# Optimization experiments

Measured on AMD Instinct MI355X. Metric: run time of the kernel, lower is better.

Reference implementation:

```python
import jax, jax.numpy as jnp
import numpy as np
from jax import lax

KH = KW = 3
DIL = 4
D = DIL * (KH - 1) + 1  # dilated (effective) kernel extent = 9
PAD = 4
STRIDE = 1


def setup_inputs() -> dict:
    key = jax.random.key(0)
    k1, k2, k3, k4 = jax.random.split(key, 4)
    Cin, Cout, B, H, W = 128, 128, 16, 112, 112
    fan_in = Cin * KH * KW
    x = jax.random.normal(k1, (B, Cin, H, W), dtype=jnp.float32)
    weight = jax.random.normal(k2, (Cout, Cin, KH, KW), dtype=jnp.float32) / np.sqrt(fan_in)
    # learnable positions: offsets of each kernel point inside the dilated kernel
    P = jax.random.normal(k3, (2, Cout, Cin, KH, KW), dtype=jnp.float32) * (DIL / 2.0)
    bias = jax.random.normal(k4, (Cout,), dtype=jnp.float32) * 0.01
    return {"x": x, "weight": weight, "P": P, "bias": bias}


def _construct_kernel(weight, P):
    # Place each kernel point at its (learnable) continuous position inside the
    # D x D dilated kernel via bilinear interpolation (DCLS construction).
    O, C, kh, kw = weight.shape
    base_h = jnp.arange(kh, dtype=weight.dtype) * DIL  # regular dilated grid
    base_w = jnp.arange(kw, dtype=weight.dtype) * DIL
    p_h = jnp.clip(base_h[None, None, :, None] + P[0], 0.0, D - 1)  # (O,C,kh,kw)
    p_w = jnp.clip(base_w[None, None, None, :] + P[1], 0.0, D - 1)
    fh = jnp.floor(p_h)
    fw = jnp.floor(p_w)
    rh = p_h - fh  # fractional residuals -> bilinear weights
    rw = p_w - fw
    ih = fh.astype(jnp.int32)
    iw = fw.astype(jnp.int32)
    ih1 = jnp.minimum(ih + 1, D - 1)
    iw1 = jnp.minimum(iw + 1, D - 1)
    o = jnp.arange(O)[:, None, None, None]
    c = jnp.arange(C)[None, :, None, None]
    K = jnp.zeros((O, C, D, D), dtype=weight.dtype)
    K = K.at[o, c, ih, iw].add(weight * (1 - rh) * (1 - rw))
    K = K.at[o, c, ih1, iw].add(weight * rh * (1 - rw))
    K = K.at[o, c, ih, iw1].add(weight * (1 - rh) * rw)
    K = K.at[o, c, ih1, iw1].add(weight * rh * rw)
    return K


def reference(x, weight, P, bias):
    K = _construct_kernel(weight, P)  # (Cout, Cin, D, D)
    out = lax.conv_general_dilated(
        x, K,
        window_strides=(STRIDE, STRIDE),
        padding=[(PAD, PAD), (PAD, PAD)],
        dimension_numbers=("NCHW", "OIHW", "NCHW"),
        feature_group_count=1,
    )
    return out + bias[None, :, None, None]
```

## Files before the change

### kernel.cpp

```cpp
#include <hip/hip_runtime.h>
#include <hip/hip_bf16.h>
#include <stdint.h>


typedef __attribute__((ext_vector_type(8))) short short8;
typedef __attribute__((ext_vector_type(16))) float f32x16;

__device__ inline unsigned short f2bf(float f) {
    union { float f; unsigned int u; } v; v.f = f;
    unsigned int u = v.u;
    return (unsigned short)((u + 0x7FFFu + ((u >> 16) & 1u)) >> 16);
}

__global__ void build_K(const float* __restrict__ weight,
                        const float* __restrict__ P,
                        unsigned short* __restrict__ Kws) {
    __shared__ float sacc[128 * 81];
    int tid = threadIdx.x;
    int o = blockIdx.x;
    int c = tid;
    float* a = &sacc[c * 81];
    for (int i = 0; i < 81; ++i) a[i] = 0.0f;
    int base = (o * 128 + c) * 9;
    #pragma unroll
    for (int kh = 0; kh < 3; ++kh) {
        #pragma unroll
        for (int kw = 0; kw < 3; ++kw) {
            int kk = kh * 3 + kw;
            float w  = weight[base + kk];
            float p0 = P[base + kk];
            float p1 = P[128 * 128 * 9 + base + kk];
            float ph = fminf(fmaxf((float)(kh * 4) + p0, 0.0f), 8.0f);
            float pw = fminf(fmaxf((float)(kw * 4) + p1, 0.0f), 8.0f);
            float fh = floorf(ph), fw = floorf(pw);
            float rh = ph - fh, rw = pw - fw;
            int ih = (int)fh, iw = (int)fw;
            int ih1 = min(ih + 1, 8), iw1 = min(iw + 1, 8);
            a[ih  * 9 + iw ] += w * (1.0f - rh) * (1.0f - rw);
            a[ih1 * 9 + iw ] += w * rh * (1.0f - rw);
            a[ih  * 9 + iw1] += w * (1.0f - rh) * rw;
            a[ih1 * 9 + iw1] += w * rh * rw;
        }
    }
    __syncthreads();
    for (int u = tid; u < 1296; u += 128) {
        int tap = u >> 4;
        int rem = u & 15;
        int chunk = rem >> 1, half = rem & 1;
        int c0 = chunk * 16 + half * 8;
        short8 v;
        #pragma unroll
        for (int j = 0; j < 8; ++j)
            v[j] = (short)f2bf(sacc[(c0 + j) * 81 + tap]);
        *(short8*)(Kws + ((tap * 8 + chunk) * 2 + half) * 1024 + o * 8) = v;
    }
}

__device__ inline void dma3(const char* Kb, char* dst, int tapbase, int cc,
                            int woff, int lane16) {
    #pragma unroll
    for (int j = 0; j < 3; ++j) {
        const char* src = Kb + (((size_t)((tapbase + j) * 8 + cc)) << 12)
                             + woff + lane16;
        __builtin_amdgcn_global_load_lds(
            (const __attribute__((address_space(1))) char*)src,
            (__attribute__((address_space(3))) char*)(dst + j * 4096 + woff),
            16, 0, 0);
    }
}

__global__ __launch_bounds__(256, 2)
void dcls_conv(const float* __restrict__ x,
               const unsigned short* __restrict__ Kws,
               const float* __restrict__ bias,
               float* __restrict__ out) {
    __shared__ __align__(16) char sX[18432];
    __shared__ __align__(16) char sK0[12288];
    __shared__ __align__(16) char sK1[12288];

    int bid = blockIdx.x;
    int b   = bid / 49;
    int rem = bid % 49;
    int ty  = rem / 7, tx = rem % 7;
    int y0  = ty * 16, x0 = tx * 16;

    int tid  = threadIdx.x;
    int lane = tid & 63;
    int wave = tid >> 6;
    int mgrp = wave >> 1;
    int ngrp = wave & 1;
    int half = lane >> 5;
    int l31  = lane & 31;
    int lrow = (lane >> 4) & 1;
    int lcol = lane & 15;
    int woff = wave * 1024;
    int lane16 = lane * 16;

    f32x16 acc[2][4];
    #pragma unroll
    for (int i = 0; i < 2; ++i)
        #pragma unroll
        for (int j = 0; j < 4; ++j)
            #pragma unroll
            for (int k = 0; k < 16; ++k) acc[i][j][k] = 0.0f;

    int preA[2];
    #pragma unroll
    for (int i = 0; i < 2; ++i)
        preA[i] = half * 2048 + ((mgrp * 2 + i) * 32 + l31) * 16;
    int preB[4];
    #pragma unroll
    for (int j = 0; j < 4; ++j)
        preB[j] = (2 * (ngrp * 4 + j) + lrow) * 768 + half * 384 + lcol * 16;

    const char* __restrict__ Kb = (const char*)Kws;

    for (int cc = 0; cc < 8; ++cc) {
        __syncthreads();
        {
            int cbase = cc * 16;
            #pragma unroll
            for (int it = 0; it < 5; ++it) {
                int u = tid + it * 256;
                if (u < 1152) {
                    int r  = u / 48;
                    int rr = u % 48;
                    int hf = rr / 24;
                    int co = rr % 24;
                    int h = y0 - 4 + r;
                    int w = x0 - 4 + co;
                    bool ok = (h >= 0) & (h < 112) & (w >= 0) & (w < 112);
                    const float* xp = x + (((b * 128 + cbase + hf * 8) * 112 + h) * 112 + w);
                    short8 v;
                    #pragma unroll
                    for (int j = 0; j < 8; ++j) {
                        float f = ok ? xp[j * 112 * 112] : 0.0f;
                        v[j] = (short)f2bf(f);
                    }
                    *(short8*)(sX + u * 16) = v;
                }
            }
        }
        __syncthreads();

        dma3(Kb, sK0, 0, cc, woff, lane16);
        dma3(Kb, sK1, 3, cc, woff, lane16);

        int tg = 0, t = 0;
        for (int g = 0; g < 27; ++g) {
            if (g < 26) {
                asm volatile("s_waitcnt vmcnt(3)\n\ts_barrier" ::: "memory");
            } else {
                asm volatile("s_waitcnt vmcnt(0)\n\ts_barrier" ::: "memory");
            }
            char* buf = (g & 1) ? sK1 : sK0;
            #pragma unroll
            for (int j = 0; j < 3; ++j) {
                int tapoff = tg * 768 + t * 16;
                short8 af[2];
                #pragma unroll
                for (int i = 0; i < 2; ++i)
                    af[i] = *(const short8*)(buf + j * 4096 + preA[i]);
                short8 bfr[4];
                #pragma unroll
                for (int jj = 0; jj < 4; ++jj)
                    bfr[jj] = *(const short8*)(sX + preB[jj] + tapoff);
                #pragma unroll
                for (int i = 0; i < 2; ++i)
                    #pragma unroll
                    for (int jj = 0; jj < 4; ++jj)
                        acc[i][jj] = __builtin_amdgcn_mfma_f32_32x32x16_bf16(
                            af[i], bfr[jj], acc[i][jj], 0, 0, 0);
                if (++t == 9) { t = 0; ++tg; }
            }
            if (g < 25) {
                asm volatile("s_barrier" ::: "memory");
                dma3(Kb, buf, (g + 2) * 3, cc, woff, lane16);
            }
        }
    }

    #pragma unroll
    for (int i = 0; i < 2; ++i) {
        int ob = (mgrp * 2 + i) * 32;
        #pragma unroll
        for (int r = 0; r < 16; ++r) {
            int o = ob + (r & 3) + 8 * (r >> 2) + 4 * half;
            float bv = bias[o];
            #pragma unroll
            for (int j = 0; j < 4; ++j) {
                int nt  = ngrp * 4 + j;
                int row = y0 + 2 * nt + lrow;
                int col = x0 + lcol;
                out[((b * 128 + o) * 112 + row) * 112 + col] = acc[i][j][r] + bv;
            }
        }
    }
}

extern "C" void kernel_launch(void* const* d_in, const int* in_sizes, int n_in,
                              void* d_out, int out_size, void* d_ws, size_t ws_size,
                              hipStream_t stream) {
    const float* x      = (const float*)d_in[0];
    const float* weight = (const float*)d_in[1];
    const float* P      = (const float*)d_in[2];
    const float* bias   = (const float*)d_in[3];
    float* out = (float*)d_out;
    unsigned short* Kws = (unsigned short*)d_ws;

    build_K<<<128, 128, 0, stream>>>(weight, P, Kws);
    dcls_conv<<<784, 256, 0, stream>>>(x, Kws, bias, out);
}
```

Baseline: 626.7 us.

## Load weight fragments directly from global into registers, drop LDS weight buffers

Replaces the double-buffered global-to-LDS DMA of the weight taps, which needed a barrier per tap group, with direct per-lane global loads of the A fragments into registers, prefetched one tap ahead. This removes 27 barriers per channel chunk and frees 24 KB of LDS per block. The cost is that each wave now issues its own global loads, and each tap has only one MFMA group to hide their latency. The weight fragments are shared across blocks, so these loads are expected to hit in L2.

```diff
diff --git a/kernel.cpp b/kernel.cpp
--- a/kernel.cpp
+++ b/kernel.cpp
@@ -56,27 +56,12 @@
     }
 }
 
-__device__ inline void dma3(const char* Kb, char* dst, int tapbase, int cc,
-                            int woff, int lane16) {
-    #pragma unroll
-    for (int j = 0; j < 3; ++j) {
-        const char* src = Kb + (((size_t)((tapbase + j) * 8 + cc)) << 12)
-                             + woff + lane16;
-        __builtin_amdgcn_global_load_lds(
-            (const __attribute__((address_space(1))) char*)src,
-            (__attribute__((address_space(3))) char*)(dst + j * 4096 + woff),
-            16, 0, 0);
-    }
-}
-
 __global__ __launch_bounds__(256, 2)
 void dcls_conv(const float* __restrict__ x,
                const unsigned short* __restrict__ Kws,
                const float* __restrict__ bias,
                float* __restrict__ out) {
     __shared__ __align__(16) char sX[18432];
-    __shared__ __align__(16) char sK0[12288];
-    __shared__ __align__(16) char sK1[12288];
 
     int bid = blockIdx.x;
     int b   = bid / 49;
@@ -93,8 +78,6 @@
     int l31  = lane & 31;
     int lrow = (lane >> 4) & 1;
     int lcol = lane & 15;
-    int woff = wave * 1024;
-    int lane16 = lane * 16;
 
     f32x16 acc[2][4];
     #pragma unroll
@@ -143,39 +126,36 @@
         }
         __syncthreads();
 
-        dma3(Kb, sK0, 0, cc, woff, lane16);
-        dma3(Kb, sK1, 3, cc, woff, lane16);
+        const char* Kc = Kb + (cc << 12);
+        short8 ca0 = *(const short8*)(Kc + preA[0]);
+        short8 ca1 = *(const short8*)(Kc + preA[1]);
+        for (int tg = 0; tg < 9; ++tg) {
+            const char* Krow = Kc + (size_t)tg * (9 * 32768);
+            int rowoff = tg * 768;
+            #pragma unroll
+            for (int t = 0; t < 9; ++t) {
+                const char* nx = Krow + (size_t)(t + 1) * 32768;
+                if (t == 8 && tg == 8) nx = Krow + (size_t)8 * 32768;
+                short8 na0 = *(const short8*)(nx + preA[0]);
+                short8 na1 = *(const short8*)(nx + preA[1]);
 
-        int tg = 0, t = 0;
-        for (int g = 0; g < 27; ++g) {
-            if (g < 26) {
-                asm volatile("s_waitcnt vmcnt(3)\n\ts_barrier" ::: "memory");
-            } else {
-                asm volatile("s_waitcnt vmcnt(0)\n\ts_barrier" ::: "memory");
-            }
-            char* buf = (g & 1) ? sK1 : sK0;
-            #pragma unroll
-            for (int j = 0; j < 3; ++j) {
-                int tapoff = tg * 768 + t * 16;
-                short8 af[2];
-                #pragma unroll
-                for (int i = 0; i < 2; ++i)
-                    af[i] = *(const short8*)(buf + j * 4096 + preA[i]);
-                short8 bfr[4];
-                #pragma unroll
-                for (int jj = 0; jj < 4; ++jj)
-                    bfr[jj] = *(const short8*)(sX + preB[jj] + tapoff);
-                #pragma unroll
-                for (int i = 0; i < 2; ++i)
-                    #pragma unroll
-                    for (int jj = 0; jj < 4; ++jj)
-                        acc[i][jj] = __builtin_amdgcn_mfma_f32_32x32x16_bf16(
-                            af[i], bfr[jj], acc[i][jj], 0, 0, 0);
-                if (++t == 9) { t = 0; ++tg; }
-            }
-            if (g < 25) {
-                asm volatile("s_barrier" ::: "memory");
-                dma3(Kb, buf, (g + 2) * 3, cc, woff, lane16);
+                int tapoff = rowoff + t * 16;
+                short8 b0 = *(const short8*)(sX + preB[0] + tapoff);
+                short8 b1 = *(const short8*)(sX + preB[1] + tapoff);
+                short8 b2 = *(const short8*)(sX + preB[2] + tapoff);
+                short8 b3 = *(const short8*)(sX + preB[3] + tapoff);
+
+                acc[0][0] = __builtin_amdgcn_mfma_f32_32x32x16_bf16(ca0, b0, acc[0][0], 0, 0, 0);
+                acc[1][0] = __builtin_amdgcn_mfma_f32_32x32x16_bf16(ca1, b0, acc[1][0], 0, 0, 0);
+                acc[0][1] = __builtin_amdgcn_mfma_f32_32x32x16_bf16(ca0, b1, acc[0][1], 0, 0, 0);
+                acc[1][1] = __builtin_amdgcn_mfma_f32_32x32x16_bf16(ca1, b1, acc[1][1], 0, 0, 0);
+                acc[0][2] = __builtin_amdgcn_mfma_f32_32x32x16_bf16(ca0, b2, acc[0][2], 0, 0, 0);
+                acc[1][2] = __builtin_amdgcn_mfma_f32_32x32x16_bf16(ca1, b2, acc[1][2], 0, 0, 0);
+                acc[0][3] = __builtin_amdgcn_mfma_f32_32x32x16_bf16(ca0, b3, acc[0][3], 0, 0, 0);
+                acc[1][3] = __builtin_amdgcn_mfma_f32_32x32x16_bf16(ca1, b3, acc[1][3], 0, 0, 0);
+
+                ca0 = na0;
+                ca1 = na1;
             }
         }
     }
```

After: 876.9 us. 39.9% more time.
